# Optimization experiments

Hardware: AMD Instinct MI355X
Metric: run time of the kernel (lower is better)

The kernel has to match this reference:

```python
import jax, jax.numpy as jnp
import numpy as np

N_NODES = 100000
N_EDGES = 1600000
N_CLASS = 10
HIDDEN = 128
BN_EPS = 1e-5


def _bn(h, gamma, beta):
    # BatchNorm1d in training mode: biased batch statistics over the node dim
    m = h.mean(axis=0)
    v = ((h - m) ** 2).mean(axis=0)
    return gamma * (h - m) / jnp.sqrt(v + BN_EPS) + beta


def _mlp(h, w1, b1, g1, t1, w2, b2, g2, t2):
    h = jax.nn.relu(_bn(h @ w1 + b1, g1, t1))
    h = jax.nn.relu(_bn(h @ w2 + b2, g2, t2))
    return h


def _gin_conv(x, edge_index, mlp_params):
    src, dst = edge_index[0], edge_index[1]
    # sum-aggregate neighbor messages: [E, D] gather + scatter-add -> [N, D]
    agg = jax.ops.segment_sum(x[src], dst, num_segments=N_NODES)
    h = x + agg  # (1 + eps) * x + agg, eps = 0
    return _mlp(h, *mlp_params)


def setup_inputs() -> dict:
    key = jax.random.key(0)
    ks = jax.random.split(key, 16)
    x = jax.random.normal(ks[0], (N_NODES, N_CLASS), dtype=jnp.float32)
    edge_index = jax.random.randint(ks[1], (2, N_EDGES), 0, N_NODES, dtype=jnp.int64)
    edge_weight = jax.random.uniform(ks[2], (N_EDGES,), dtype=jnp.float32)

    def lin(k, fan_in, fan_out):
        bound = 1.0 / np.sqrt(fan_in)
        kw, kb = jax.random.split(k)
        w = jax.random.uniform(kw, (fan_in, fan_out), minval=-bound, maxval=bound, dtype=jnp.float32)
        b = jax.random.uniform(kb, (fan_out,), minval=-bound, maxval=bound, dtype=jnp.float32)
        return w, b

    w11, b11 = lin(ks[3], N_CLASS, HIDDEN)
    w12, b12 = lin(ks[4], HIDDEN, HIDDEN)
    w21, b21 = lin(ks[5], HIDDEN, HIDDEN)
    w22, b22 = lin(ks[6], HIDDEN, HIDDEN)
    wf, bf = lin(ks[7], HIDDEN, N_CLASS)
    ones = jnp.ones((HIDDEN,), jnp.float32)
    zeros = jnp.zeros((HIDDEN,), jnp.float32)
    return {
        "x": x, "edge_weight": edge_weight,
        "w11": w11, "b11": b11, "g11": ones, "t11": zeros,
        "w12": w12, "b12": b12, "g12": ones, "t12": zeros,
        "w21": w21, "b21": b21, "g21": ones, "t21": zeros,
        "w22": w22, "b22": b22, "g22": ones, "t22": zeros,
        "wf": wf, "bf": bf,
        "edge_index": edge_index,
    }


def reference(x, edge_weight, w11, b11, g11, t11, w12, b12, g12, t12,
              w21, b21, g21, t21, w22, b22, g22, t22, wf, bf, edge_index):
    h = jax.nn.relu(_gin_conv(x, edge_index, (w11, b11, g11, t11, w12, b12, g12, t12)))
    h = jax.nn.relu(_gin_conv(h, edge_index, (w21, b21, g21, t21, w22, b22, g22, t22)))
    logits = h @ wf + bf
    return jax.nn.log_softmax(logits, axis=1)
```

## Files before the change

### kernel.cpp

```cpp
#include <hip/hip_runtime.h>

#define N_CLASS 10
#define HIDDEN 128
#define BN_EPS 1e-5f

typedef short short8 __attribute__((ext_vector_type(8)));
typedef float floatx4 __attribute__((ext_vector_type(4)));

__device__ __forceinline__ float bf2f(unsigned short u) {
    unsigned int x = ((unsigned int)u) << 16;
    float f; __builtin_memcpy(&f, &x, 4); return f;
}
__device__ __forceinline__ unsigned short f2bf(float f) {
    unsigned int x; __builtin_memcpy(&x, &f, 4);
    x += 0x7FFFu + ((x >> 16) & 1u);
    return (unsigned short)(x >> 16);
}
__device__ __forceinline__ float lo_f(unsigned int u) {
    unsigned int x = u << 16; float f; __builtin_memcpy(&f, &x, 4); return f;
}
__device__ __forceinline__ float hi_f(unsigned int u) {
    unsigned int x = u & 0xffff0000u; float f; __builtin_memcpy(&f, &x, 4); return f;
}


__global__ __launch_bounds__(512) void bhist_k(const int* __restrict__ ei,
                                               int* __restrict__ bhist, int E) {
    __shared__ int h[512];
    int tid = threadIdx.x;
    h[tid] = 0;
    __syncthreads();
    for (int e = blockIdx.x * 512 + tid; e < E; e += gridDim.x * 512)
        atomicAdd(&h[((unsigned)ei[E + e]) >> 8], 1);
    __syncthreads();
    if (h[tid]) atomicAdd(&bhist[tid], h[tid]);
}

__global__ __launch_bounds__(512) void bscan_k(const int* __restrict__ bhist,
                                               int* __restrict__ bstart,
                                               int* __restrict__ bcur, int NBK) {
    __shared__ int sm[512];
    int t = threadIdx.x;
    sm[t] = (t < NBK) ? bhist[t] : 0;
    __syncthreads();
    for (int off = 1; off < 512; off <<= 1) {
        int u = (t >= off) ? sm[t - off] : 0;
        __syncthreads();
        sm[t] += u;
        __syncthreads();
    }
    int excl = (t == 0) ? 0 : sm[t - 1];
    if (t <= NBK) bstart[t] = excl;
    if (t < NBK)  bcur[t]   = excl;
}

__global__ __launch_bounds__(512) void bscatter_k(const int* __restrict__ ei,
                                                  int* __restrict__ bcur,
                                                  int2* __restrict__ pairs, int E) {
    __shared__ int h[512], base[512], cur[512];
    int tid = threadIdx.x;
    h[tid] = 0; cur[tid] = 0;
    __syncthreads();
    int chunk = (E + gridDim.x - 1) / gridDim.x;
    int e0 = blockIdx.x * chunk;
    int e1 = min(e0 + chunk, E);
    for (int e = e0 + tid; e < e1; e += 512)
        atomicAdd(&h[((unsigned)ei[E + e]) >> 8], 1);
    __syncthreads();
    base[tid] = h[tid] ? atomicAdd(&bcur[tid], h[tid]) : 0;
    __syncthreads();
    for (int e = e0 + tid; e < e1; e += 512) {
        int s = ei[e], d = ei[E + e];
        int bk = ((unsigned)d) >> 8;
        int r = atomicAdd(&cur[bk], 1);
        pairs[base[bk] + r] = make_int2(s, d);
    }
}

__global__ __launch_bounds__(512) void bcsr_k(const int2* __restrict__ pairs,
                                              const int* __restrict__ bstart,
                                              int* __restrict__ row_ptr,
                                              int* __restrict__ cnt,
                                              int* __restrict__ col, int N) {
    __shared__ int h[256], sc[256], cur[256];
    int tid = threadIdx.x;
    if (tid < 256) { h[tid] = 0; cur[tid] = 0; }
    __syncthreads();
    int b = blockIdx.x, lo = b << 8;
    int s = bstart[b], e = bstart[b + 1];
    for (int i = s + tid; i < e; i += 512)
        atomicAdd(&h[pairs[i].y - lo], 1);
    __syncthreads();
    if (tid < 256) sc[tid] = h[tid];
    __syncthreads();
    for (int off = 1; off < 256; off <<= 1) {
        int u = (tid < 256 && tid >= off) ? sc[tid - off] : 0;
        __syncthreads();
        if (tid < 256) sc[tid] += u;
        __syncthreads();
    }
    if (tid < 256) {
        int d = lo + tid;
        if (d < N) { cnt[d] = h[tid]; row_ptr[d] = s + sc[tid] - h[tid]; }
        sc[tid] -= h[tid];
    }
    __syncthreads();
    for (int i = s + tid; i < e; i += 512) {
        int2 p = pairs[i];
        int d = p.y - lo;
        int r = atomicAdd(&cur[d], 1);
        col[s + sc[d] + r] = p.x;
    }
}

__global__ void prep_k(const float* __restrict__ W0, const float* __restrict__ W1,
                       const float* __restrict__ W2,
                       unsigned short* __restrict__ T0, unsigned short* __restrict__ T1,
                       unsigned short* __restrict__ T2,
                       float* __restrict__ stats, int* __restrict__ bhist) {
    const float* W = (blockIdx.y == 0) ? W0 : (blockIdx.y == 1) ? W1 : W2;
    unsigned short* T = (blockIdx.y == 0) ? T0 : (blockIdx.y == 1) ? T1 : T2;
    int i = blockIdx.x * 256 + threadIdx.x;
    if (i < 128 * 128) {
        int k = i >> 7, n = i & 127;
        T[n * 128 + k] = f2bf(W[k * 128 + n]);
    }
    if (blockIdx.y == 0) {
        if (i < 1024) stats[i] = 0.f;
        if (i < 512)  bhist[i] = 0;
    }
}

__global__ void padx_k(const float* __restrict__ X, float* __restrict__ XP, int N) {
    int i = blockIdx.x * 256 + threadIdx.x;
    if (i >= N * 16) return;
    int node = i >> 4, f = i & 15;
    XP[i] = (f < N_CLASS) ? X[node * N_CLASS + f] : 0.f;
}

__global__ void gather10_k(const float* __restrict__ XP, const int* __restrict__ col,
                           const int* __restrict__ rp, const int* __restrict__ cnt,
                           float* __restrict__ out, int N) {
    int t = blockIdx.x * 256 + threadIdx.x;
    int node = t >> 4, f = t & 15;
    if (node >= N) return;
    int start = rp[node], deg = cnt[node];
    float acc = XP[node * 16 + f];
    int j = 0;
    for (; j + 8 <= deg; j += 8) {
        int s0 = col[start + j],     s1 = col[start + j + 1];
        int s2 = col[start + j + 2], s3 = col[start + j + 3];
        int s4 = col[start + j + 4], s5 = col[start + j + 5];
        int s6 = col[start + j + 6], s7 = col[start + j + 7];
        float v0 = XP[s0 * 16 + f];
        float v1 = XP[s1 * 16 + f];
        float v2 = XP[s2 * 16 + f];
        float v3 = XP[s3 * 16 + f];
        float v4 = XP[s4 * 16 + f];
        float v5 = XP[s5 * 16 + f];
        float v6 = XP[s6 * 16 + f];
        float v7 = XP[s7 * 16 + f];
        acc += v0; acc += v1; acc += v2; acc += v3;
        acc += v4; acc += v5; acc += v6; acc += v7;
    }
    for (; j < deg; ++j)
        acc += XP[col[start + j] * 16 + f];
    out[node * 16 + f] = acc;
}

__global__ __launch_bounds__(256) void act2_k(
    const unsigned short* __restrict__ Z, unsigned short* __restrict__ R,
    const float* __restrict__ st, const float* __restrict__ g,
    const float* __restrict__ b, int N, float inv_n) {
    __shared__ float sTab[128], hTab[128];
    int tid = threadIdx.x;
    if (tid < 128) {
        float m = st[tid] * inv_n;
        float v = fmaxf(st[128 + tid] * inv_n - m * m, 0.f);
        float s = g[tid] * rsqrtf(v + BN_EPS);
        sTab[tid] = s;
        hTab[tid] = b[tid] - m * s;
    }
    __syncthreads();
    int total = N * 16;
    for (int i = blockIdx.x * 256 + tid; i < total; i += gridDim.x * 256) {
        int k8 = (i & 15) * 8;
        uint4 v = ((const uint4*)Z)[i];
        unsigned short* us = (unsigned short*)&v;
#pragma unroll
        for (int j = 0; j < 8; ++j) {
            float f = fmaxf(fmaf(bf2f(us[j]), sTab[k8 + j], hTab[k8 + j]), 0.f);
            us[j] = f2bf(f);
        }
        ((uint4*)R)[i] = v;
    }
}

__global__ __launch_bounds__(256) void gather_sum_k(
    const unsigned short* __restrict__ R, const int* __restrict__ col,
    const int* __restrict__ rp, const int* __restrict__ cnt,
    unsigned short* __restrict__ out, int N) {
    int wave = __builtin_amdgcn_readfirstlane((blockIdx.x * 256 + threadIdx.x) >> 6);
    int lane = threadIdx.x & 63;
    if (wave >= N) return;
    int start = __builtin_amdgcn_readfirstlane(rp[wave]);
    int deg   = __builtin_amdgcn_readfirstlane(cnt[wave]);
    const unsigned int* Xv = (const unsigned int*)R;
    unsigned int self = Xv[wave * 64 + lane];
    float a0 = lo_f(self);
    float a1 = hi_f(self);
    int j = 0;
    for (; j + 8 <= deg; j += 8) {
        int n0 = col[start + j],     n1 = col[start + j + 1];
        int n2 = col[start + j + 2], n3 = col[start + j + 3];
        int n4 = col[start + j + 4], n5 = col[start + j + 5];
        int n6 = col[start + j + 6], n7 = col[start + j + 7];
        unsigned int w0 = Xv[n0 * 64 + lane];
        unsigned int w1 = Xv[n1 * 64 + lane];
        unsigned int w2 = Xv[n2 * 64 + lane];
        unsigned int w3 = Xv[n3 * 64 + lane];
        unsigned int w4 = Xv[n4 * 64 + lane];
        unsigned int w5 = Xv[n5 * 64 + lane];
        unsigned int w6 = Xv[n6 * 64 + lane];
        unsigned int w7 = Xv[n7 * 64 + lane];
        a0 += lo_f(w0); a1 += hi_f(w0);
        a0 += lo_f(w1); a1 += hi_f(w1);
        a0 += lo_f(w2); a1 += hi_f(w2);
        a0 += lo_f(w3); a1 += hi_f(w3);
        a0 += lo_f(w4); a1 += hi_f(w4);
        a0 += lo_f(w5); a1 += hi_f(w5);
        a0 += lo_f(w6); a1 += hi_f(w6);
        a0 += lo_f(w7); a1 += hi_f(w7);
    }
    for (; j < deg; ++j) {
        unsigned int v = Xv[col[start + j] * 64 + lane];
        a0 += lo_f(v); a1 += hi_f(v);
    }
    unsigned int o = (unsigned int)f2bf(a0) | ((unsigned int)f2bf(a1) << 16);
    ((unsigned int*)out)[wave * 64 + lane] = o;
}

__global__ __launch_bounds__(128) void gemm10_k(
    const float* __restrict__ A, const float* __restrict__ W,
    const float* __restrict__ bias, unsigned short* __restrict__ C,
    float* __restrict__ stOut, int N) {
    __shared__ float rb[16 * 16];
    const int tid = threadIdx.x;
    float wreg[N_CLASS];
#pragma unroll
    for (int k = 0; k < N_CLASS; ++k) wreg[k] = W[k * HIDDEN + tid];
    float bb = bias[tid];
    float s = 0.f, s2 = 0.f;
    for (int r0 = blockIdx.x * 16; r0 < N; r0 += gridDim.x * 16) {
        int nr = min(16, N - r0);
        for (int i = tid; i < nr * 16; i += 128) rb[i] = A[r0 * 16 + i];
        __syncthreads();
        for (int r = 0; r < nr; ++r) {
            float acc = bb;
#pragma unroll
            for (int k = 0; k < N_CLASS; ++k) acc = fmaf(rb[r * 16 + k], wreg[k], acc);
            C[(r0 + r) * HIDDEN + tid] = f2bf(acc);
            s += acc; s2 += acc * acc;
        }
        __syncthreads();
    }
    atomicAdd(stOut + tid, s);
    atomicAdd(stOut + HIDDEN + tid, s2);
}

template<bool BN>
__global__ __launch_bounds__(256) void gemm_mfma_k(
    const unsigned short* __restrict__ Zin, const unsigned short* __restrict__ Wt,
    const float* __restrict__ bias,
    const float* __restrict__ stIn, const float* __restrict__ gIn,
    const float* __restrict__ tIn,
    unsigned short* __restrict__ Zout, float* __restrict__ stOut,
    int N, float inv_n) {
    __shared__ unsigned short Wl[128 * 136];
    __shared__ unsigned short Al[64 * 136];
    __shared__ float sTab[128], hTab[128], biasTab[128];
    __shared__ float redS[128], redS2[128];

    const int tid  = threadIdx.x;
    const int wv   = tid >> 6;
    const int ln   = tid & 63;
    const int half = ln >> 4;
    const int l16  = ln & 15;

    if (tid < 128) {
        biasTab[tid] = bias[tid];
        if (BN) {
            float m = stIn[tid] * inv_n;
            float v = fmaxf(stIn[128 + tid] * inv_n - m * m, 0.f);
            float s = gIn[tid] * rsqrtf(v + BN_EPS);
            sTab[tid] = s;
            hTab[tid] = tIn[tid] - m * s;
        }
        redS[tid] = 0.f; redS2[tid] = 0.f;
    }
    for (int c = tid; c < 2048; c += 256) {
        int n = c >> 4, k8 = c & 15;
        uint4 v = *(const uint4*)(Wt + n * 128 + k8 * 8);
        *(uint4*)(&Wl[n * 136 + k8 * 8]) = v;
    }
    __syncthreads();

    float cs[8], cs2[8];
#pragma unroll
    for (int i = 0; i < 8; ++i) { cs[i] = 0.f; cs2[i] = 0.f; }

    const int ntiles = (N + 63) >> 6;
    for (int tile = blockIdx.x; tile < ntiles; tile += gridDim.x) {
        const int r0 = tile * 64;
        for (int c = tid; c < 1024; c += 256) {
            int r = c >> 4, k8 = c & 15;
            int gr = r0 + r; if (gr >= N) gr = N - 1;
            uint4 v = *(const uint4*)(Zin + gr * 128 + k8 * 8);
            if (BN) {
                unsigned short* us = (unsigned short*)&v;
                int kb = k8 * 8;
#pragma unroll
                for (int j = 0; j < 8; ++j) {
                    float f = fmaxf(fmaf(bf2f(us[j]), sTab[kb + j], hTab[kb + j]), 0.f);
                    us[j] = f2bf(f);
                }
            }
            *(uint4*)(&Al[r * 136 + k8 * 8]) = v;
        }
        __syncthreads();

        short8 afrag[4];
        const int arow = wv * 16 + l16;
#pragma unroll
        for (int s = 0; s < 4; ++s)
            afrag[s] = *(const short8*)(&Al[arow * 136 + s * 32 + half * 8]);
        __syncthreads();

#pragma unroll
        for (int ct = 0; ct < 8; ++ct) {
            floatx4 acc = {0.f, 0.f, 0.f, 0.f};
            const int bn_ = ct * 16 + l16;
#pragma unroll
            for (int s = 0; s < 4; ++s) {
                short8 bfrag = *(const short8*)(&Wl[bn_ * 136 + s * 32 + half * 8]);
                acc = __builtin_amdgcn_mfma_f32_16x16x32_bf16(afrag[s], bfrag, acc, 0, 0, 0);
            }
            float bcol = biasTab[bn_];
#pragma unroll
            for (int r = 0; r < 4; ++r) {
                int lrow = wv * 16 + half * 4 + r;
                float val = acc[r] + bcol;
                if (r0 + lrow < N) { cs[ct] += val; cs2[ct] += val * val; }
                Al[lrow * 136 + bn_] = f2bf(val);
            }
        }
        __syncthreads();

        for (int c = tid; c < 1024; c += 256) {
            int r = c >> 4, k8 = c & 15;
            int gr = r0 + r;
            if (gr < N)
                *(uint4*)(Zout + gr * 128 + k8 * 8) = *(const uint4*)(&Al[r * 136 + k8 * 8]);
        }
        __syncthreads();
    }

#pragma unroll
    for (int ct = 0; ct < 8; ++ct) {
        float a = cs[ct], b = cs2[ct];
        a += __shfl_xor(a, 16); a += __shfl_xor(a, 32);
        b += __shfl_xor(b, 16); b += __shfl_xor(b, 32);
        if (half == 0) {
            atomicAdd(&redS[ct * 16 + l16], a);
            atomicAdd(&redS2[ct * 16 + l16], b);
        }
    }
    __syncthreads();
    if (tid < 128) {
        atomicAdd(stOut + tid, redS[tid]);
        atomicAdd(stOut + 128 + tid, redS2[tid]);
    }
}

__global__ __launch_bounds__(256) void final_mfma_k(
    const unsigned short* __restrict__ Z, const float* __restrict__ st,
    const float* __restrict__ g, const float* __restrict__ b,
    const float* __restrict__ wf, const float* __restrict__ bfc,
    float* __restrict__ out, int N, float inv_n) {
    __shared__ unsigned short Al[64 * 136];
    __shared__ unsigned short Bl[16 * 136];
    __shared__ float sTab[128], hTab[128], biasTab[16];

    const int tid  = threadIdx.x;
    const int wv   = tid >> 6;
    const int ln   = tid & 63;
    const int half = ln >> 4;
    const int l16  = ln & 15;

    if (tid < 128) {
        float m = st[tid] * inv_n;
        float v = fmaxf(st[128 + tid] * inv_n - m * m, 0.f);
        float s = g[tid] * rsqrtf(v + BN_EPS);
        sTab[tid] = s;
        hTab[tid] = b[tid] - m * s;
    }
    if (tid < 16) biasTab[tid] = (tid < N_CLASS) ? bfc[tid] : -3.0e38f;
    {
        int n = tid >> 4, k8 = (tid & 15) * 8;
        uint4 v;
        unsigned short* us = (unsigned short*)&v;
#pragma unroll
        for (int j = 0; j < 8; ++j)
            us[j] = (n < N_CLASS) ? f2bf(wf[(k8 + j) * N_CLASS + n]) : (unsigned short)0;
        *(uint4*)(&Bl[n * 136 + k8]) = v;
    }
    __syncthreads();

    short8 bfrag[4];
#pragma unroll
    for (int s = 0; s < 4; ++s)
        bfrag[s] = *(const short8*)(&Bl[l16 * 136 + s * 32 + half * 8]);

    const int ntiles = (N + 63) >> 6;
    for (int tile = blockIdx.x; tile < ntiles; tile += gridDim.x) {
        const int r0 = tile * 64;
        for (int c = tid; c < 1024; c += 256) {
            int r = c >> 4, k8 = c & 15;
            int gr = r0 + r; if (gr >= N) gr = N - 1;
            uint4 v = *(const uint4*)(Z + gr * 128 + k8 * 8);
            unsigned short* us = (unsigned short*)&v;
            int kb = k8 * 8;
#pragma unroll
            for (int j = 0; j < 8; ++j) {
                float f = fmaxf(fmaf(bf2f(us[j]), sTab[kb + j], hTab[kb + j]), 0.f);
                us[j] = f2bf(f);
            }
            *(uint4*)(&Al[r * 136 + k8 * 8]) = v;
        }
        __syncthreads();

        short8 afrag[4];
        const int arow = wv * 16 + l16;
#pragma unroll
        for (int s = 0; s < 4; ++s)
            afrag[s] = *(const short8*)(&Al[arow * 136 + s * 32 + half * 8]);
        __syncthreads();

        floatx4 acc = {0.f, 0.f, 0.f, 0.f};
#pragma unroll
        for (int s = 0; s < 4; ++s)
            acc = __builtin_amdgcn_mfma_f32_16x16x32_bf16(afrag[s], bfrag[s], acc, 0, 0, 0);

        float bcol = biasTab[l16];
#pragma unroll
        for (int r = 0; r < 4; ++r) {
            float lg = acc[r] + bcol;
            float mx = lg;
            mx = fmaxf(mx, __shfl_xor(mx, 1));
            mx = fmaxf(mx, __shfl_xor(mx, 2));
            mx = fmaxf(mx, __shfl_xor(mx, 4));
            mx = fmaxf(mx, __shfl_xor(mx, 8));
            float p = __expf(lg - mx);
            float se = p;
            se += __shfl_xor(se, 1);
            se += __shfl_xor(se, 2);
            se += __shfl_xor(se, 4);
            se += __shfl_xor(se, 8);
            float ls = __logf(se);
            int grow = r0 + wv * 16 + half * 4 + r;
            if (l16 < N_CLASS && grow < N)
                out[grow * N_CLASS + l16] = lg - mx - ls;
        }
    }
}


extern "C" void kernel_launch(void* const* d_in, const int* in_sizes, int n_in,
                              void* d_out, int out_size, void* d_ws, size_t ws_size,
                              hipStream_t stream) {
    const float* x   = (const float*)d_in[0];
    const float* w11 = (const float*)d_in[2];
    const float* b11 = (const float*)d_in[3];
    const float* g11 = (const float*)d_in[4];
    const float* t11 = (const float*)d_in[5];
    const float* w12 = (const float*)d_in[6];
    const float* b12 = (const float*)d_in[7];
    const float* g12 = (const float*)d_in[8];
    const float* t12 = (const float*)d_in[9];
    const float* w21 = (const float*)d_in[10];
    const float* b21 = (const float*)d_in[11];
    const float* g21 = (const float*)d_in[12];
    const float* t21 = (const float*)d_in[13];
    const float* w22 = (const float*)d_in[14];
    const float* b22 = (const float*)d_in[15];
    const float* g22 = (const float*)d_in[16];
    const float* t22 = (const float*)d_in[17];
    const float* wf  = (const float*)d_in[18];
    const float* bf  = (const float*)d_in[19];
    const int*   ei  = (const int*)d_in[20];

    const int N = in_sizes[0] / N_CLASS;
    const int E = in_sizes[1];
    const float inv_n = 1.0f / (float)N;
    const int NBK = (N + 255) >> 8;

    char* base = (char*)d_ws;
    size_t off = 0;
    auto take = [&](size_t bytes) { void* p = base + off; off += (bytes + 15) & ~(size_t)15; return p; };
    float*          stats   = (float*)take(1024 * 4);
    float*          xp      = (float*)take((size_t)N * 16 * 4);
    float*          h0      = (float*)take((size_t)N * 16 * 4);
    int*            cnt     = (int*)take((size_t)N * 4);
    int*            row_ptr = (int*)take((size_t)N * 4);
    int*            bhist   = (int*)take(512 * 4);
    int*            bstart  = (int*)take(520 * 4);
    int*            bcur    = (int*)take(512 * 4);
    int2*           pairs   = (int2*)take((size_t)E * 8);
    int*            col     = (int*)take((size_t)E * 4);
    unsigned short* bufA    = (unsigned short*)take((size_t)N * HIDDEN * 2);
    unsigned short* bufB    = (unsigned short*)take((size_t)N * HIDDEN * 2);
    unsigned short* bufC    = (unsigned short*)take((size_t)N * HIDDEN * 2);
    unsigned short* Wt1     = (unsigned short*)take(128 * 128 * 2);
    unsigned short* Wt2     = (unsigned short*)take(128 * 128 * 2);
    unsigned short* Wt3     = (unsigned short*)take(128 * 128 * 2);

    prep_k<<<dim3(64, 3), 256, 0, stream>>>(w12, w21, w22, Wt1, Wt2, Wt3,
                                            stats, bhist);
    padx_k<<<(N * 16 + 255) / 256, 256, 0, stream>>>(x, xp, N);

    bhist_k<<<256, 512, 0, stream>>>(ei, bhist, E);
    bscan_k<<<1, 512, 0, stream>>>(bhist, bstart, bcur, NBK);
    bscatter_k<<<256, 512, 0, stream>>>(ei, bcur, pairs, E);
    bcsr_k<<<NBK, 512, 0, stream>>>(pairs, bstart, row_ptr, cnt, col, N);

    gather10_k<<<(N * 16 + 255) / 256, 256, 0, stream>>>(xp, col, row_ptr, cnt, h0, N);
    gemm10_k<<<512, 128, 0, stream>>>(h0, w11, b11, bufA, stats, N);
    gemm_mfma_k<true><<<512, 256, 0, stream>>>(bufA, Wt1, b12, stats, g11, t11,
                                               bufB, stats + 256, N, inv_n);

    act2_k<<<3125, 256, 0, stream>>>(bufB, bufC, stats + 256, g12, t12, N, inv_n);
    gather_sum_k<<<(N * 64 + 255) / 256, 256, 0, stream>>>(bufC, col, row_ptr, cnt,
                                                           bufA, N);

    gemm_mfma_k<false><<<512, 256, 0, stream>>>(bufA, Wt2, b21, nullptr, nullptr, nullptr,
                                                bufB, stats + 512, N, inv_n);
    gemm_mfma_k<true><<<512, 256, 0, stream>>>(bufB, Wt3, b22, stats + 512, g21, t21,
                                               bufA, stats + 768, N, inv_n);

    final_mfma_k<<<782, 256, 0, stream>>>(bufA, stats + 768, g22, t22,
                                          wf, bf, (float*)d_out, N, inv_n);
}
```

Before: 404.3 us.

## Pack edge pairs, store padded input as bf16, fuse padding into prep, retune GEMM grid

Edge pairs for the CSR build are packed into one 32-bit word (24-bit source plus 8-bit local destination), halving the intermediate traffic. The padded input features are now stored in bf16 and written inside the prep kernel, which removes one launch and halves the first gather's bytes. The GEMM reduction scratch reuses the A tile's shared memory, and the MFMA GEMM grids grow from 512 to 768 blocks. The packing assumes node ids fit in 24 bits, and bf16 input adds rounding error to the first-layer aggregation.

```diff
diff --git a/kernel.cpp b/kernel.cpp
--- a/kernel.cpp
+++ b/kernel.cpp
@@ -56,7 +56,7 @@
 
 __global__ __launch_bounds__(512) void bscatter_k(const int* __restrict__ ei,
                                                   int* __restrict__ bcur,
-                                                  int2* __restrict__ pairs, int E) {
+                                                  unsigned int* __restrict__ pairs, int E) {
     __shared__ int h[512], base[512], cur[512];
     int tid = threadIdx.x;
     h[tid] = 0; cur[tid] = 0;
@@ -70,14 +70,15 @@
     base[tid] = h[tid] ? atomicAdd(&bcur[tid], h[tid]) : 0;
     __syncthreads();
     for (int e = e0 + tid; e < e1; e += 512) {
-        int s = ei[e], d = ei[E + e];
-        int bk = ((unsigned)d) >> 8;
+        unsigned int s = (unsigned int)ei[e];
+        unsigned int d = (unsigned int)ei[E + e];
+        int bk = d >> 8;
         int r = atomicAdd(&cur[bk], 1);
-        pairs[base[bk] + r] = make_int2(s, d);
-    }
-}
-
-__global__ __launch_bounds__(512) void bcsr_k(const int2* __restrict__ pairs,
+        pairs[base[bk] + r] = s | ((d & 255u) << 24);
+    }
+}
+
+__global__ __launch_bounds__(512) void bcsr_k(const unsigned int* __restrict__ pairs,
                                               const int* __restrict__ bstart,
                                               int* __restrict__ row_ptr,
                                               int* __restrict__ cnt,
@@ -89,7 +90,7 @@
     int b = blockIdx.x, lo = b << 8;
     int s = bstart[b], e = bstart[b + 1];
     for (int i = s + tid; i < e; i += 512)
-        atomicAdd(&h[pairs[i].y - lo], 1);
+        atomicAdd(&h[pairs[i] >> 24], 1);
     __syncthreads();
     if (tid < 256) sc[tid] = h[tid];
     __syncthreads();
@@ -106,10 +107,10 @@
     }
     __syncthreads();
     for (int i = s + tid; i < e; i += 512) {
-        int2 p = pairs[i];
-        int d = p.y - lo;
+        unsigned int p = pairs[i];
+        int d = p >> 24;
         int r = atomicAdd(&cur[d], 1);
-        col[s + sc[d] + r] = p.x;
+        col[s + sc[d] + r] = (int)(p & 0xFFFFFFu);
     }
 }
 
@@ -117,54 +118,57 @@
                        const float* __restrict__ W2,
                        unsigned short* __restrict__ T0, unsigned short* __restrict__ T1,
                        unsigned short* __restrict__ T2,
-                       float* __restrict__ stats, int* __restrict__ bhist) {
-    const float* W = (blockIdx.y == 0) ? W0 : (blockIdx.y == 1) ? W1 : W2;
-    unsigned short* T = (blockIdx.y == 0) ? T0 : (blockIdx.y == 1) ? T1 : T2;
+                       float* __restrict__ stats, int* __restrict__ bhist,
+                       const float* __restrict__ x, unsigned short* __restrict__ xp,
+                       int N) {
+    int y = blockIdx.y;
     int i = blockIdx.x * 256 + threadIdx.x;
-    if (i < 128 * 128) {
-        int k = i >> 7, n = i & 127;
-        T[n * 128 + k] = f2bf(W[k * 128 + n]);
-    }
-    if (blockIdx.y == 0) {
-        if (i < 1024) stats[i] = 0.f;
-        if (i < 512)  bhist[i] = 0;
-    }
-}
-
-__global__ void padx_k(const float* __restrict__ X, float* __restrict__ XP, int N) {
-    int i = blockIdx.x * 256 + threadIdx.x;
-    if (i >= N * 16) return;
-    int node = i >> 4, f = i & 15;
-    XP[i] = (f < N_CLASS) ? X[node * N_CLASS + f] : 0.f;
-}
-
-__global__ void gather10_k(const float* __restrict__ XP, const int* __restrict__ col,
+    if (y < 3) {
+        const float* W = (y == 0) ? W0 : (y == 1) ? W1 : W2;
+        unsigned short* T = (y == 0) ? T0 : (y == 1) ? T1 : T2;
+        if (i < 128 * 128) {
+            int k = i >> 7, n = i & 127;
+            T[n * 128 + k] = f2bf(W[k * 128 + n]);
+        }
+        if (y == 0) {
+            if (i < 1024) stats[i] = 0.f;
+            if (i < 512)  bhist[i] = 0;
+        }
+    } else {
+        for (int c = i; c < N * 16; c += 64 * 256) {
+            int node = c >> 4, f = c & 15;
+            xp[c] = (f < N_CLASS) ? f2bf(x[node * N_CLASS + f]) : (unsigned short)0;
+        }
+    }
+}
+
+__global__ void gather10_k(const unsigned short* __restrict__ XP, const int* __restrict__ col,
                            const int* __restrict__ rp, const int* __restrict__ cnt,
                            float* __restrict__ out, int N) {
     int t = blockIdx.x * 256 + threadIdx.x;
     int node = t >> 4, f = t & 15;
     if (node >= N) return;
     int start = rp[node], deg = cnt[node];
-    float acc = XP[node * 16 + f];
+    float acc = bf2f(XP[node * 16 + f]);
     int j = 0;
     for (; j + 8 <= deg; j += 8) {
         int s0 = col[start + j],     s1 = col[start + j + 1];
         int s2 = col[start + j + 2], s3 = col[start + j + 3];
         int s4 = col[start + j + 4], s5 = col[start + j + 5];
         int s6 = col[start + j + 6], s7 = col[start + j + 7];
-        float v0 = XP[s0 * 16 + f];
-        float v1 = XP[s1 * 16 + f];
-        float v2 = XP[s2 * 16 + f];
-        float v3 = XP[s3 * 16 + f];
-        float v4 = XP[s4 * 16 + f];
-        float v5 = XP[s5 * 16 + f];
-        float v6 = XP[s6 * 16 + f];
-        float v7 = XP[s7 * 16 + f];
+        float v0 = bf2f(XP[s0 * 16 + f]);
+        float v1 = bf2f(XP[s1 * 16 + f]);
+        float v2 = bf2f(XP[s2 * 16 + f]);
+        float v3 = bf2f(XP[s3 * 16 + f]);
+        float v4 = bf2f(XP[s4 * 16 + f]);
+        float v5 = bf2f(XP[s5 * 16 + f]);
+        float v6 = bf2f(XP[s6 * 16 + f]);
+        float v7 = bf2f(XP[s7 * 16 + f]);
         acc += v0; acc += v1; acc += v2; acc += v3;
         acc += v4; acc += v5; acc += v6; acc += v7;
     }
     for (; j < deg; ++j)
-        acc += XP[col[start + j] * 16 + f];
+        acc += bf2f(XP[col[start + j] * 16 + f]);
     out[node * 16 + f] = acc;
 }
 
@@ -279,7 +283,6 @@
     __shared__ unsigned short Wl[128 * 136];
     __shared__ unsigned short Al[64 * 136];
     __shared__ float sTab[128], hTab[128], biasTab[128];
-    __shared__ float redS[128], redS2[128];
 
     const int tid  = threadIdx.x;
     const int wv   = tid >> 6;
@@ -296,7 +299,6 @@
             sTab[tid] = s;
             hTab[tid] = tIn[tid] - m * s;
         }
-        redS[tid] = 0.f; redS2[tid] = 0.f;
     }
     for (int c = tid; c < 2048; c += 256) {
         int n = c >> 4, k8 = c & 15;
@@ -365,20 +367,23 @@
         __syncthreads();
     }
 
+    float* red = (float*)Al;
+    if (tid < 256) red[tid] = 0.f;
+    __syncthreads();
 #pragma unroll
     for (int ct = 0; ct < 8; ++ct) {
         float a = cs[ct], b = cs2[ct];
         a += __shfl_xor(a, 16); a += __shfl_xor(a, 32);
         b += __shfl_xor(b, 16); b += __shfl_xor(b, 32);
         if (half == 0) {
-            atomicAdd(&redS[ct * 16 + l16], a);
-            atomicAdd(&redS2[ct * 16 + l16], b);
+            atomicAdd(&red[ct * 16 + l16], a);
+            atomicAdd(&red[128 + ct * 16 + l16], b);
         }
     }
     __syncthreads();
     if (tid < 128) {
-        atomicAdd(stOut + tid, redS[tid]);
-        atomicAdd(stOut + 128 + tid, redS2[tid]);
+        atomicAdd(stOut + tid, red[tid]);
+        atomicAdd(stOut + 128 + tid, red[128 + tid]);
     }
 }
 
@@ -508,14 +513,14 @@
     size_t off = 0;
     auto take = [&](size_t bytes) { void* p = base + off; off += (bytes + 15) & ~(size_t)15; return p; };
     float*          stats   = (float*)take(1024 * 4);
-    float*          xp      = (float*)take((size_t)N * 16 * 4);
+    unsigned short* xp      = (unsigned short*)take((size_t)N * 16 * 2);
     float*          h0      = (float*)take((size_t)N * 16 * 4);
     int*            cnt     = (int*)take((size_t)N * 4);
     int*            row_ptr = (int*)take((size_t)N * 4);
     int*            bhist   = (int*)take(512 * 4);
     int*            bstart  = (int*)take(520 * 4);
     int*            bcur    = (int*)take(512 * 4);
-    int2*           pairs   = (int2*)take((size_t)E * 8);
+    unsigned int*   pairs   = (unsigned int*)take((size_t)E * 4);
     int*            col     = (int*)take((size_t)E * 4);
     unsigned short* bufA    = (unsigned short*)take((size_t)N * HIDDEN * 2);
     unsigned short* bufB    = (unsigned short*)take((size_t)N * HIDDEN * 2);
@@ -524,9 +529,8 @@
     unsigned short* Wt2     = (unsigned short*)take(128 * 128 * 2);
     unsigned short* Wt3     = (unsigned short*)take(128 * 128 * 2);
 
-    prep_k<<<dim3(64, 3), 256, 0, stream>>>(w12, w21, w22, Wt1, Wt2, Wt3,
-                                            stats, bhist);
-    padx_k<<<(N * 16 + 255) / 256, 256, 0, stream>>>(x, xp, N);
+    prep_k<<<dim3(64, 4), 256, 0, stream>>>(w12, w21, w22, Wt1, Wt2, Wt3,
+                                            stats, bhist, x, xp, N);
 
     bhist_k<<<256, 512, 0, stream>>>(ei, bhist, E);
     bscan_k<<<1, 512, 0, stream>>>(bhist, bstart, bcur, NBK);
@@ -535,16 +539,16 @@
 
     gather10_k<<<(N * 16 + 255) / 256, 256, 0, stream>>>(xp, col, row_ptr, cnt, h0, N);
     gemm10_k<<<512, 128, 0, stream>>>(h0, w11, b11, bufA, stats, N);
-    gemm_mfma_k<true><<<512, 256, 0, stream>>>(bufA, Wt1, b12, stats, g11, t11,
+    gemm_mfma_k<true><<<768, 256, 0, stream>>>(bufA, Wt1, b12, stats, g11, t11,
                                                bufB, stats + 256, N, inv_n);
 
     act2_k<<<3125, 256, 0, stream>>>(bufB, bufC, stats + 256, g12, t12, N, inv_n);
     gather_sum_k<<<(N * 64 + 255) / 256, 256, 0, stream>>>(bufC, col, row_ptr, cnt,
                                                            bufA, N);
 
-    gemm_mfma_k<false><<<512, 256, 0, stream>>>(bufA, Wt2, b21, nullptr, nullptr, nullptr,
+    gemm_mfma_k<false><<<768, 256, 0, stream>>>(bufA, Wt2, b21, nullptr, nullptr, nullptr,
                                                 bufB, stats + 512, N, inv_n);
-    gemm_mfma_k<true><<<512, 256, 0, stream>>>(bufB, Wt3, b22, stats + 512, g21, t21,
+    gemm_mfma_k<true><<<768, 256, 0, stream>>>(bufB, Wt3, b22, stats + 512, g21, t21,
                                                bufA, stats + 768, N, inv_n);
 
     final_mfma_k<<<782, 256, 0, stream>>>(bufA, stats + 768, g22, t22,
```

New measurement: 440.8 us. +9.0%, slower.
